# Optimization experiments

Measured on AMD Instinct MI355X. Metric: run time of the kernel, lower is better.

## Reference

```python
import jax, jax.numpy as jnp
import numpy as np

N = 1024      # number of spans
D = 512       # span embedding dim (input_dim = 3*D)
H = 150       # hidden_dim
WIN = 250     # antecedent window from spans[ix-250:ix]


def setup_inputs() -> dict:
    key = jax.random.key(0)
    ks = jax.random.split(key, 8)
    return {
        "g": jax.random.normal(ks[0], (N, D), jnp.float32),
        "sm": jax.random.normal(ks[1], (N,), jnp.float32),
        "W1": jax.random.normal(ks[2], (3 * D, H), jnp.float32) * (1.0 / np.sqrt(3 * D)),
        "b1": jax.random.normal(ks[3], (H,), jnp.float32) * 0.01,
        "W2": jax.random.normal(ks[4], (H, H), jnp.float32) * (1.0 / np.sqrt(H)),
        "b2": jax.random.normal(ks[5], (H,), jnp.float32) * 0.01,
        "W3": jax.random.normal(ks[6], (H, 1), jnp.float32) * (1.0 / np.sqrt(H)),
        "b3": jax.random.normal(ks[7], (1,), jnp.float32) * 0.01,
    }


def reference(g, sm, W1, b1, W2, b2, W3, b3):
    n, d = g.shape
    # matching the in-order iteration over spans[ix-250:ix]
    j = jnp.arange(n)[:, None] - WIN + jnp.arange(WIN)[None, :]
    valid = j >= 0
    jc = jnp.clip(j, 0)

    # pair feature is cat([g_i, g_j, g_i*g_j]); split W1 so we can factor the first GEMM
    W1a, W1b, W1c = jnp.split(W1, 3, axis=0)            # each [D, H]
    gi_term = g @ W1a                                    # [N, H]
    gj_term = (g @ W1b)[jc]
    prod_term = jnp.einsum('nwd,dh->nwh', g[:, None, :] * g[jc], W1c)

    h = jax.nn.relu(gi_term[:, None, :] + gj_term + prod_term + b1)
    h = jax.nn.relu(h @ W2 + b2)
    s = (h @ W3 + b3)[..., 0]

    sij = sm[:, None] + sm[jc] + s                       # sm_i + sm_j + s_a
    sij = jnp.where(valid, sij, 0.0)                     # mask out-of-range antecedents
    eps = jnp.zeros((n, 1), g.dtype)                     # trailing epsilon = 0
    return jnp.concatenate([sij, eps], axis=1)
```

## Files before the change

### kernel.cpp

```cpp
#include <hip/hip_runtime.h>

typedef __attribute__((ext_vector_type(8))) short short8;
typedef __attribute__((ext_vector_type(4))) float f32x4;

#define NSPAN 1024
#define DDIM  512
#define HDIM  150
#define HPAD  160
#define WINW  250
#define OUTW  251

#define B1_OFF0 0
#define B1_OFF1 10240
#define SL_OFF  40960
#define SMEM_BYTES 41472

__device__ __forceinline__ unsigned short f2bf(float x) {
  union { float f; unsigned int u; } v; v.f = x;
  return (unsigned short)((v.u + 0x7fffu + ((v.u >> 16) & 1u)) >> 16);
}

__device__ __forceinline__ unsigned int cvtpk(float a, float b) {
  unsigned int r;
  asm("v_cvt_pk_bf16_f32 %0, %1, %2" : "=v"(r) : "v"(a), "v"(b));
  return r;
}

__device__ __forceinline__ void gload_lds16(const void* g, void* l) {
  __builtin_amdgcn_global_load_lds(
      (const __attribute__((address_space(1))) unsigned int*)g,
      (__attribute__((address_space(3))) unsigned int*)l, 16, 0, 0);
}

__global__ __launch_bounds__(192) void prep_gemm(
    const float* __restrict__ g, const float* __restrict__ W1,
    const float* __restrict__ b1, float* __restrict__ pre1,
    float* __restrict__ gjb)
{
  __shared__ __align__(16) float gs[2 * DDIM];
  const int grp = blockIdx.x >> 1;
  const int which = blockIdx.x & 1;
  const int i0 = grp << 1;
  for (int idx = threadIdx.x; idx < (2 * DDIM / 4); idx += 192)
    ((float4*)gs)[idx] = ((const float4*)(g + (size_t)i0 * DDIM))[idx];
  __syncthreads();
  const int n = threadIdx.x;
  float a0 = 0.f, a1 = 0.f;
  if (n < HDIM) {
    const float* Wp = W1 + (size_t)which * DDIM * HDIM + n;
#pragma unroll 8
    for (int d = 0; d < DDIM; ++d) {
      float w = Wp[(size_t)d * HDIM];
      a0 += gs[d] * w;
      a1 += gs[DDIM + d] * w;
    }
  }
  if (n < HPAD) {
    float* dst = which ? gjb : pre1;
    float add = (which == 0 && n < HDIM) ? b1[n] : 0.f;
    float v0 = (n < HDIM) ? (a0 + add) : 0.f;
    float v1 = (n < HDIM) ? (a1 + add) : 0.f;
    dst[(size_t)i0 * HPAD + n] = v0;
    dst[(size_t)(i0 + 1) * HPAD + n] = v1;
  }
}

__global__ void prep_misc(const float* __restrict__ W1, const float* __restrict__ W2,
                          const float* __restrict__ W3,
                          unsigned short* __restrict__ w1cT,
                          unsigned short* __restrict__ w2T,
                          float* __restrict__ w3p)
{
  int id = blockIdx.x * 256 + threadIdx.x;
  if (id < HPAD * DDIM) {
    int d = id / HPAD, n = id % HPAD;
    float v = (n < HDIM) ? W1[(size_t)(2 * DDIM + d) * HDIM + n] : 0.f;
    w1cT[(size_t)n * DDIM + d] = f2bf(v);
  } else if (id < HPAD * DDIM + HPAD * HPAD) {
    int id2 = id - HPAD * DDIM;
    int k = id2 / HPAD, n = id2 % HPAD;
    float v = (n < HDIM && k < HDIM) ? W2[(size_t)k * HDIM + n] : 0.f;
    w2T[(size_t)n * HPAD + k] = f2bf(v);
  } else if (id < HPAD * DDIM + HPAD * HPAD + HPAD) {
    int n = id - HPAD * DDIM - HPAD * HPAD;
    w3p[n] = (n < HDIM) ? W3[n] : 0.f;
  }
}

__global__ __launch_bounds__(256, 3) void pair_main(
    const float* __restrict__ g, const float* __restrict__ sm,
    const float* __restrict__ pre1, const float* __restrict__ gjb,
    const unsigned short* __restrict__ w1cT, const unsigned short* __restrict__ w2T,
    const float* __restrict__ w3p, const float* __restrict__ b2,
    const float* __restrict__ b3, float* __restrict__ out)
{
  __shared__ __align__(16) char smem[SMEM_BYTES];
  const int tid = threadIdx.x;
  const int lane = tid & 63;
  const int wv = tid >> 6;
  const int l15 = lane & 15;
  const int lq = lane >> 4;
  const int i = blockIdx.x >> 1;
  const int mbase = (blockIdx.x & 1) << 7;

  const int row0 = mbase + (wv << 5) + l15;
  int j0 = i - WINW + row0;
  j0 = j0 < 0 ? 0 : (j0 > NSPAN - 1 ? NSPAN - 1 : j0);
  int j1 = i - WINW + row0 + 16;
  j1 = j1 < 0 ? 0 : (j1 > NSPAN - 1 ? NSPAN - 1 : j1);
  const float* gjr0 = g + (size_t)j0 * DDIM + (lq << 3);
  const float* gjr1 = g + (size_t)j1 * DDIM + (lq << 3);
  const float* giR  = g + (size_t)i * DDIM + (lq << 3);

  unsigned int bsrc[3];
#pragma unroll
  for (int t = 0; t < 3; ++t) {
    int b = wv * 2560 + (t << 10) + (lane << 4);
    int m = b >> 7;
    int bp = b ^ ((m & 7) << 4);
    int n = bp >> 6, o = bp & 63;
    bsrc[t] = (unsigned int)(n * 1024 + o);
  }

  int xb[10];
#pragma unroll
  for (int nt = 0; nt < 10; ++nt) {
    int nr = (nt << 4) + l15;
    xb[nt] = ((nr << 6) + (lq << 4)) ^ (((nr >> 1) & 7) << 4);
  }

  f32x4 acc[2][10];
#pragma unroll
  for (int mt = 0; mt < 2; ++mt)
#pragma unroll
    for (int nt = 0; nt < 10; ++nt)
      acc[mt][nt] = (f32x4){0.f, 0.f, 0.f, 0.f};

  const char* w1cB = (const char*)w1cT;

  {
    char* ldsw = smem + B1_OFF0 + wv * 2560;
    gload_lds16(w1cB + bsrc[0], ldsw);
    gload_lds16(w1cB + bsrc[1], ldsw + 1024);
    if (lane < 32) gload_lds16(w1cB + bsrc[2], ldsw + 2048);
  }
  uint4 aC0, aC1;
  {
    float4 x0 = *(const float4*)gjr0, x1 = *(const float4*)(gjr0 + 4);
    float4 y0 = *(const float4*)gjr1, y1 = *(const float4*)(gjr1 + 4);
    float4 g0 = *(const float4*)giR,  g1 = *(const float4*)(giR + 4);
    aC0.x = cvtpk(x0.x * g0.x, x0.y * g0.y);
    aC0.y = cvtpk(x0.z * g0.z, x0.w * g0.w);
    aC0.z = cvtpk(x1.x * g1.x, x1.y * g1.y);
    aC0.w = cvtpk(x1.z * g1.z, x1.w * g1.w);
    aC1.x = cvtpk(y0.x * g0.x, y0.y * g0.y);
    aC1.y = cvtpk(y0.z * g0.z, y0.w * g0.w);
    aC1.z = cvtpk(y1.x * g1.x, y1.y * g1.y);
    aC1.w = cvtpk(y1.z * g1.z, y1.w * g1.w);
  }
  __syncthreads();

#pragma unroll 2
  for (int s = 0; s < 16; ++s) {
    char* bcur = smem + ((s & 1) ? B1_OFF1 : B1_OFF0);
    char* bnxt = smem + ((s & 1) ? B1_OFF0 : B1_OFF1);

    if (s < 15) {
      const int kn = (s + 1) << 6;
      char* ldsw = bnxt + wv * 2560;
      gload_lds16(w1cB + bsrc[0] + kn, ldsw);
      gload_lds16(w1cB + bsrc[1] + kn, ldsw + 1024);
      if (lane < 32) gload_lds16(w1cB + bsrc[2] + kn, ldsw + 2048);
    }
    float4 x0, x1, y0, y1, g0, g1;
    if (s < 15) {
      const int kf = (s + 1) << 5;
      x0 = *(const float4*)(gjr0 + kf); x1 = *(const float4*)(gjr0 + kf + 4);
      y0 = *(const float4*)(gjr1 + kf); y1 = *(const float4*)(gjr1 + kf + 4);
      g0 = *(const float4*)(giR + kf);  g1 = *(const float4*)(giR + kf + 4);
    }
    short8 a0 = *(short8*)&aC0;
    short8 a1 = *(short8*)&aC1;
#pragma unroll
    for (int nt = 0; nt < 10; ++nt) {
      short8 bb = *(const short8*)(bcur + xb[nt]);
      acc[0][nt] = __builtin_amdgcn_mfma_f32_16x16x32_bf16(a0, bb, acc[0][nt], 0, 0, 0);
      acc[1][nt] = __builtin_amdgcn_mfma_f32_16x16x32_bf16(a1, bb, acc[1][nt], 0, 0, 0);
    }
    if (s < 15) {
      aC0.x = cvtpk(x0.x * g0.x, x0.y * g0.y);
      aC0.y = cvtpk(x0.z * g0.z, x0.w * g0.w);
      aC0.z = cvtpk(x1.x * g1.x, x1.y * g1.y);
      aC0.w = cvtpk(x1.z * g1.z, x1.w * g1.w);
      aC1.x = cvtpk(y0.x * g0.x, y0.y * g0.y);
      aC1.y = cvtpk(y0.z * g0.z, y0.w * g0.w);
      aC1.z = cvtpk(y1.x * g1.x, y1.y * g1.y);
      aC1.w = cvtpk(y1.z * g1.z, y1.w * g1.w);
    }
    __syncthreads();
  }

  float p1v[10];
#pragma unroll
  for (int nt = 0; nt < 10; ++nt)
    p1v[nt] = pre1[(size_t)i * HPAD + (nt << 4) + l15];

#pragma unroll
  for (int mt = 0; mt < 2; ++mt) {
#pragma unroll
    for (int rr = 0; rr < 4; ++rr) {
      const int row = (wv << 5) + (mt << 4) + (lq << 2) + rr;
      int j = i - WINW + mbase + row;
      j = j < 0 ? 0 : (j > NSPAN - 1 ? NSPAN - 1 : j);
      const float* gjr = gjb + (size_t)j * HPAD;
      const int sw = ((row + (row >> 2)) & 3) << 4;
      const int rb = row * 320;
#pragma unroll
      for (int np = 0; np < 5; ++np) {
        const int n0 = np << 1, n1 = n0 + 1;
        float v0 = fmaxf(acc[mt][n0][rr] + p1v[n0] + gjr[(n0 << 4) + l15], 0.f);
        float v1 = fmaxf(acc[mt][n1][rr] + p1v[n1] + gjr[(n1 << 4) + l15], 0.f);
        unsigned int u = cvtpk(v0, v1);
        *(unsigned short*)(smem + ((rb + (((n0 << 4) + l15) << 1)) ^ sw)) = (unsigned short)u;
        *(unsigned short*)(smem + ((rb + (((n1 << 4) + l15) << 1)) ^ sw)) = (unsigned short)(u >> 16);
      }
    }
  }

  int ya[2];
#pragma unroll
  for (int mt = 0; mt < 2; ++mt) {
    int row = (wv << 5) + (mt << 4) + l15;
    ya[mt] = ((row * 320) + (lq << 4)) ^ (((row + (row >> 2)) & 3) << 4);
  }

#pragma unroll
  for (int mt = 0; mt < 2; ++mt)
#pragma unroll
    for (int nt = 0; nt < 10; ++nt)
      acc[mt][nt] = (f32x4){0.f, 0.f, 0.f, 0.f};

#pragma unroll
  for (int c = 0; c < 5; ++c) {
    short8 a0 = *(const short8*)(smem + ya[0] + (c << 6));
    short8 a1 = *(const short8*)(smem + ya[1] + (c << 6));
#pragma unroll
    for (int nt = 0; nt < 10; ++nt) {
      short8 bb = *(const short8*)(w2T + (size_t)((nt << 4) + l15) * HPAD + (c << 5) + (lq << 3));
      acc[0][nt] = __builtin_amdgcn_mfma_f32_16x16x32_bf16(a0, bb, acc[0][nt], 0, 0, 0);
      acc[1][nt] = __builtin_amdgcn_mfma_f32_16x16x32_bf16(a1, bb, acc[1][nt], 0, 0, 0);
    }
  }

  float w3v[10], b2v[10];
#pragma unroll
  for (int nt = 0; nt < 10; ++nt) {
    int nn = (nt << 4) + l15;
    w3v[nt] = w3p[nn];
    b2v[nt] = (nn < HDIM) ? b2[nn] : 0.f;
  }
  float* sL = (float*)(smem + SL_OFF);
#pragma unroll
  for (int mt = 0; mt < 2; ++mt) {
#pragma unroll
    for (int rr = 0; rr < 4; ++rr) {
      float part = 0.f;
#pragma unroll
      for (int nt = 0; nt < 10; ++nt) {
        float h2 = fmaxf(acc[mt][nt][rr] + b2v[nt], 0.f);
        part = fmaf(h2, w3v[nt], part);
      }
      part += __shfl_xor(part, 1);
      part += __shfl_xor(part, 2);
      part += __shfl_xor(part, 4);
      part += __shfl_xor(part, 8);
      if (l15 == 0)
        sL[(wv << 5) + (mt << 4) + (lq << 2) + rr] = part;
    }
  }
  __syncthreads();

  if (tid < 128) {
    const int rg = mbase + tid;
    if (rg <= WINW) {
      const int j = i - WINW + rg;
      float v = 0.f;
      if (rg < WINW && j >= 0)
        v = sL[tid] + b3[0] + sm[i] + sm[j];
      out[(size_t)i * OUTW + rg] = v;
    }
  }
}

extern "C" void kernel_launch(void* const* d_in, const int* in_sizes, int n_in,
                              void* d_out, int out_size, void* d_ws, size_t ws_size,
                              hipStream_t stream) {
  const float* g  = (const float*)d_in[0];
  const float* sm = (const float*)d_in[1];
  const float* W1 = (const float*)d_in[2];
  const float* b1 = (const float*)d_in[3];
  const float* W2 = (const float*)d_in[4];
  const float* b2 = (const float*)d_in[5];
  const float* W3 = (const float*)d_in[6];
  const float* b3 = (const float*)d_in[7];
  float* out = (float*)d_out;

  char* ws = (char*)d_ws;
  float* pre1          = (float*)ws;
  float* gjb           = (float*)(ws + 655360);
  unsigned short* w1cT = (unsigned short*)(ws + 1310720);
  unsigned short* w2T  = (unsigned short*)(ws + 1474560);
  float* w3p           = (float*)(ws + 1525760);

  prep_gemm<<<1024, 192, 0, stream>>>(g, W1, b1, pre1, gjb);
  prep_misc<<<(HPAD * DDIM + HPAD * HPAD + HPAD + 255) / 256, 256, 0, stream>>>(
      W1, W2, W3, w1cT, w2T, w3p);
  pair_main<<<2048, 256, 0, stream>>>(g, sm, pre1, gjb, w1cT, w2T, w3p, b2, b3, out);
}
```

Baseline: 209.7 us.

## Read W1c B-fragments directly from global and merge prep kernels into one launch

```diff
diff --git a/kernel.cpp b/kernel.cpp
--- a/kernel.cpp
+++ b/kernel.cpp
@@ -10,8 +10,6 @@
 #define WINW  250
 #define OUTW  251
 
-#define B1_OFF0 0
-#define B1_OFF1 10240
 #define SL_OFF  40960
 #define SMEM_BYTES 41472
 
@@ -26,64 +24,55 @@
   return r;
 }
 
-__device__ __forceinline__ void gload_lds16(const void* g, void* l) {
-  __builtin_amdgcn_global_load_lds(
-      (const __attribute__((address_space(1))) unsigned int*)g,
-      (__attribute__((address_space(3))) unsigned int*)l, 16, 0, 0);
-}
-
-__global__ __launch_bounds__(192) void prep_gemm(
+__global__ __launch_bounds__(192) void prep_all(
     const float* __restrict__ g, const float* __restrict__ W1,
-    const float* __restrict__ b1, float* __restrict__ pre1,
-    float* __restrict__ gjb)
+    const float* __restrict__ b1, const float* __restrict__ W2,
+    const float* __restrict__ W3,
+    float* __restrict__ pre1, float* __restrict__ gjb,
+    unsigned short* __restrict__ w1cT, unsigned short* __restrict__ w2T,
+    float* __restrict__ w3p)
 {
-  __shared__ __align__(16) float gs[2 * DDIM];
-  const int grp = blockIdx.x >> 1;
-  const int which = blockIdx.x & 1;
-  const int i0 = grp << 1;
-  for (int idx = threadIdx.x; idx < (2 * DDIM / 4); idx += 192)
-    ((float4*)gs)[idx] = ((const float4*)(g + (size_t)i0 * DDIM))[idx];
-  __syncthreads();
-  const int n = threadIdx.x;
-  float a0 = 0.f, a1 = 0.f;
-  if (n < HDIM) {
-    const float* Wp = W1 + (size_t)which * DDIM * HDIM + n;
+  const int bx = blockIdx.x;
+  if (bx < 1024) {
+    __shared__ __align__(16) float gs[2 * DDIM];
+    const int grp = bx >> 1;
+    const int which = bx & 1;
+    const int i0 = grp << 1;
+    for (int idx = threadIdx.x; idx < (2 * DDIM / 4); idx += 192)
+      ((float4*)gs)[idx] = ((const float4*)(g + (size_t)i0 * DDIM))[idx];
+    __syncthreads();
+    const int n = threadIdx.x;
+    float a0 = 0.f, a1 = 0.f;
+    if (n < HDIM) {
+      const float* Wp = W1 + (size_t)which * DDIM * HDIM + n;
 #pragma unroll 8
-    for (int d = 0; d < DDIM; ++d) {
-      float w = Wp[(size_t)d * HDIM];
-      a0 += gs[d] * w;
-      a1 += gs[DDIM + d] * w;
-    }
-  }
-  if (n < HPAD) {
-    float* dst = which ? gjb : pre1;
-    float add = (which == 0 && n < HDIM) ? b1[n] : 0.f;
-    float v0 = (n < HDIM) ? (a0 + add) : 0.f;
-    float v1 = (n < HDIM) ? (a1 + add) : 0.f;
-    dst[(size_t)i0 * HPAD + n] = v0;
-    dst[(size_t)(i0 + 1) * HPAD + n] = v1;
-  }
-}
-
-__global__ void prep_misc(const float* __restrict__ W1, const float* __restrict__ W2,
-                          const float* __restrict__ W3,
-                          unsigned short* __restrict__ w1cT,
-                          unsigned short* __restrict__ w2T,
-                          float* __restrict__ w3p)
-{
-  int id = blockIdx.x * 256 + threadIdx.x;
-  if (id < HPAD * DDIM) {
-    int d = id / HPAD, n = id % HPAD;
-    float v = (n < HDIM) ? W1[(size_t)(2 * DDIM + d) * HDIM + n] : 0.f;
-    w1cT[(size_t)n * DDIM + d] = f2bf(v);
-  } else if (id < HPAD * DDIM + HPAD * HPAD) {
-    int id2 = id - HPAD * DDIM;
-    int k = id2 / HPAD, n = id2 % HPAD;
-    float v = (n < HDIM && k < HDIM) ? W2[(size_t)k * HDIM + n] : 0.f;
-    w2T[(size_t)n * HPAD + k] = f2bf(v);
-  } else if (id < HPAD * DDIM + HPAD * HPAD + HPAD) {
-    int n = id - HPAD * DDIM - HPAD * HPAD;
-    w3p[n] = (n < HDIM) ? W3[n] : 0.f;
+      for (int d = 0; d < DDIM; ++d) {
+        float w = Wp[(size_t)d * HDIM];
+        a0 += gs[d] * w;
+        a1 += gs[DDIM + d] * w;
+      }
+    }
+    if (n < HPAD) {
+      float* dst = which ? gjb : pre1;
+      float add = (which == 0 && n < HDIM) ? b1[n] : 0.f;
+      dst[(size_t)i0 * HPAD + n]       = (n < HDIM) ? (a0 + add) : 0.f;
+      dst[(size_t)(i0 + 1) * HPAD + n] = (n < HDIM) ? (a1 + add) : 0.f;
+    }
+  } else {
+    int id = (bx - 1024) * 192 + threadIdx.x;
+    if (id < HPAD * DDIM) {
+      int d = id / HPAD, n = id % HPAD;
+      float v = (n < HDIM) ? W1[(size_t)(2 * DDIM + d) * HDIM + n] : 0.f;
+      w1cT[(size_t)n * DDIM + d] = f2bf(v);
+    } else if (id < HPAD * DDIM + HPAD * HPAD) {
+      int id2 = id - HPAD * DDIM;
+      int k = id2 / HPAD, n = id2 % HPAD;
+      float v = (n < HDIM && k < HDIM) ? W2[(size_t)k * HDIM + n] : 0.f;
+      w2T[(size_t)n * HPAD + k] = f2bf(v);
+    } else if (id < HPAD * DDIM + HPAD * HPAD + HPAD) {
+      int n = id - HPAD * DDIM - HPAD * HPAD;
+      w3p[n] = (n < HDIM) ? W3[n] : 0.f;
+    }
   }
 }
 
@@ -112,22 +101,7 @@
   const float* gjr1 = g + (size_t)j1 * DDIM + (lq << 3);
   const float* giR  = g + (size_t)i * DDIM + (lq << 3);
 
-  unsigned int bsrc[3];
-#pragma unroll
-  for (int t = 0; t < 3; ++t) {
-    int b = wv * 2560 + (t << 10) + (lane << 4);
-    int m = b >> 7;
-    int bp = b ^ ((m & 7) << 4);
-    int n = bp >> 6, o = bp & 63;
-    bsrc[t] = (unsigned int)(n * 1024 + o);
-  }
-
-  int xb[10];
-#pragma unroll
-  for (int nt = 0; nt < 10; ++nt) {
-    int nr = (nt << 4) + l15;
-    xb[nt] = ((nr << 6) + (lq << 4)) ^ (((nr >> 1) & 7) << 4);
-  }
+  const unsigned short* bB = w1cT + (size_t)l15 * DDIM + (lq << 3);
 
   f32x4 acc[2][10];
 #pragma unroll
@@ -136,19 +110,13 @@
     for (int nt = 0; nt < 10; ++nt)
       acc[mt][nt] = (f32x4){0.f, 0.f, 0.f, 0.f};
 
-  const char* w1cB = (const char*)w1cT;
-
-  {
-    char* ldsw = smem + B1_OFF0 + wv * 2560;
-    gload_lds16(w1cB + bsrc[0], ldsw);
-    gload_lds16(w1cB + bsrc[1], ldsw + 1024);
-    if (lane < 32) gload_lds16(w1cB + bsrc[2], ldsw + 2048);
-  }
-  uint4 aC0, aC1;
-  {
-    float4 x0 = *(const float4*)gjr0, x1 = *(const float4*)(gjr0 + 4);
-    float4 y0 = *(const float4*)gjr1, y1 = *(const float4*)(gjr1 + 4);
-    float4 g0 = *(const float4*)giR,  g1 = *(const float4*)(giR + 4);
+#pragma unroll 2
+  for (int s = 0; s < 16; ++s) {
+    const int kf = s << 5;
+    float4 x0 = *(const float4*)(gjr0 + kf), x1 = *(const float4*)(gjr0 + kf + 4);
+    float4 y0 = *(const float4*)(gjr1 + kf), y1 = *(const float4*)(gjr1 + kf + 4);
+    float4 g0 = *(const float4*)(giR + kf),  g1 = *(const float4*)(giR + kf + 4);
+    uint4 aC0, aC1;
     aC0.x = cvtpk(x0.x * g0.x, x0.y * g0.y);
     aC0.y = cvtpk(x0.z * g0.z, x0.w * g0.w);
     aC0.z = cvtpk(x1.x * g1.x, x1.y * g1.y);
@@ -157,47 +125,14 @@
     aC1.y = cvtpk(y0.z * g0.z, y0.w * g0.w);
     aC1.z = cvtpk(y1.x * g1.x, y1.y * g1.y);
     aC1.w = cvtpk(y1.z * g1.z, y1.w * g1.w);
-  }
-  __syncthreads();
-
-#pragma unroll 2
-  for (int s = 0; s < 16; ++s) {
-    char* bcur = smem + ((s & 1) ? B1_OFF1 : B1_OFF0);
-    char* bnxt = smem + ((s & 1) ? B1_OFF0 : B1_OFF1);
-
-    if (s < 15) {
-      const int kn = (s + 1) << 6;
-      char* ldsw = bnxt + wv * 2560;
-      gload_lds16(w1cB + bsrc[0] + kn, ldsw);
-      gload_lds16(w1cB + bsrc[1] + kn, ldsw + 1024);
-      if (lane < 32) gload_lds16(w1cB + bsrc[2] + kn, ldsw + 2048);
-    }
-    float4 x0, x1, y0, y1, g0, g1;
-    if (s < 15) {
-      const int kf = (s + 1) << 5;
-      x0 = *(const float4*)(gjr0 + kf); x1 = *(const float4*)(gjr0 + kf + 4);
-      y0 = *(const float4*)(gjr1 + kf); y1 = *(const float4*)(gjr1 + kf + 4);
-      g0 = *(const float4*)(giR + kf);  g1 = *(const float4*)(giR + kf + 4);
-    }
     short8 a0 = *(short8*)&aC0;
     short8 a1 = *(short8*)&aC1;
 #pragma unroll
     for (int nt = 0; nt < 10; ++nt) {
-      short8 bb = *(const short8*)(bcur + xb[nt]);
+      short8 bb = *(const short8*)(bB + nt * 16 * DDIM + kf);
       acc[0][nt] = __builtin_amdgcn_mfma_f32_16x16x32_bf16(a0, bb, acc[0][nt], 0, 0, 0);
       acc[1][nt] = __builtin_amdgcn_mfma_f32_16x16x32_bf16(a1, bb, acc[1][nt], 0, 0, 0);
     }
-    if (s < 15) {
-      aC0.x = cvtpk(x0.x * g0.x, x0.y * g0.y);
-      aC0.y = cvtpk(x0.z * g0.z, x0.w * g0.w);
-      aC0.z = cvtpk(x1.x * g1.x, x1.y * g1.y);
-      aC0.w = cvtpk(x1.z * g1.z, x1.w * g1.w);
-      aC1.x = cvtpk(y0.x * g0.x, y0.y * g0.y);
-      aC1.y = cvtpk(y0.z * g0.z, y0.w * g0.w);
-      aC1.z = cvtpk(y1.x * g1.x, y1.y * g1.y);
-      aC1.w = cvtpk(y1.z * g1.z, y1.w * g1.w);
-    }
-    __syncthreads();
   }
 
   float p1v[10];
@@ -312,8 +247,6 @@
   unsigned short* w2T  = (unsigned short*)(ws + 1474560);
   float* w3p           = (float*)(ws + 1525760);
 
-  prep_gemm<<<1024, 192, 0, stream>>>(g, W1, b1, pre1, gjb);
-  prep_misc<<<(HPAD * DDIM + HPAD * HPAD + HPAD + 255) / 256, 256, 0, stream>>>(
-      W1, W2, W3, w1cT, w2T, w3p);
+  prep_all<<<1585, 192, 0, stream>>>(g, W1, b1, W2, W3, pre1, gjb, w1cT, w2T, w3p);
   pair_main<<<2048, 256, 0, stream>>>(g, sm, pre1, gjb, w1cT, w2T, w3p, b2, b3, out);
 }
```

After: 354.3 us. +69.0%, slower.

## Triple-buffer W1c LDS staging with one barrier per step and merge prep kernels

Applied to the files above, without the earlier changes.

```diff
diff --git a/kernel.cpp b/kernel.cpp
--- a/kernel.cpp
+++ b/kernel.cpp
@@ -10,8 +10,6 @@
 #define WINW  250
 #define OUTW  251
 
-#define B1_OFF0 0
-#define B1_OFF1 10240
 #define SL_OFF  40960
 #define SMEM_BYTES 41472
 
@@ -32,58 +30,55 @@
       (__attribute__((address_space(3))) unsigned int*)l, 16, 0, 0);
 }
 
-__global__ __launch_bounds__(192) void prep_gemm(
+__global__ __launch_bounds__(192) void prep_all(
     const float* __restrict__ g, const float* __restrict__ W1,
-    const float* __restrict__ b1, float* __restrict__ pre1,
-    float* __restrict__ gjb)
+    const float* __restrict__ b1, const float* __restrict__ W2,
+    const float* __restrict__ W3,
+    float* __restrict__ pre1, float* __restrict__ gjb,
+    unsigned short* __restrict__ w1cT, unsigned short* __restrict__ w2T,
+    float* __restrict__ w3p)
 {
-  __shared__ __align__(16) float gs[2 * DDIM];
-  const int grp = blockIdx.x >> 1;
-  const int which = blockIdx.x & 1;
-  const int i0 = grp << 1;
-  for (int idx = threadIdx.x; idx < (2 * DDIM / 4); idx += 192)
-    ((float4*)gs)[idx] = ((const float4*)(g + (size_t)i0 * DDIM))[idx];
-  __syncthreads();
-  const int n = threadIdx.x;
-  float a0 = 0.f, a1 = 0.f;
-  if (n < HDIM) {
-    const float* Wp = W1 + (size_t)which * DDIM * HDIM + n;
+  const int bx = blockIdx.x;
+  if (bx < 1024) {
+    __shared__ __align__(16) float gs[2 * DDIM];
+    const int grp = bx >> 1;
+    const int which = bx & 1;
+    const int i0 = grp << 1;
+    for (int idx = threadIdx.x; idx < (2 * DDIM / 4); idx += 192)
+      ((float4*)gs)[idx] = ((const float4*)(g + (size_t)i0 * DDIM))[idx];
+    __syncthreads();
+    const int n = threadIdx.x;
+    float a0 = 0.f, a1 = 0.f;
+    if (n < HDIM) {
+      const float* Wp = W1 + (size_t)which * DDIM * HDIM + n;
 #pragma unroll 8
-    for (int d = 0; d < DDIM; ++d) {
-      float w = Wp[(size_t)d * HDIM];
-      a0 += gs[d] * w;
-      a1 += gs[DDIM + d] * w;
-    }
-  }
-  if (n < HPAD) {
-    float* dst = which ? gjb : pre1;
-    float add = (which == 0 && n < HDIM) ? b1[n] : 0.f;
-    float v0 = (n < HDIM) ? (a0 + add) : 0.f;
-    float v1 = (n < HDIM) ? (a1 + add) : 0.f;
-    dst[(size_t)i0 * HPAD + n] = v0;
-    dst[(size_t)(i0 + 1) * HPAD + n] = v1;
-  }
-}
-
-__global__ void prep_misc(const float* __restrict__ W1, const float* __restrict__ W2,
-                          const float* __restrict__ W3,
-                          unsigned short* __restrict__ w1cT,
-                          unsigned short* __restrict__ w2T,
-                          float* __restrict__ w3p)
-{
-  int id = blockIdx.x * 256 + threadIdx.x;
-  if (id < HPAD * DDIM) {
-    int d = id / HPAD, n = id % HPAD;
-    float v = (n < HDIM) ? W1[(size_t)(2 * DDIM + d) * HDIM + n] : 0.f;
-    w1cT[(size_t)n * DDIM + d] = f2bf(v);
-  } else if (id < HPAD * DDIM + HPAD * HPAD) {
-    int id2 = id - HPAD * DDIM;
-    int k = id2 / HPAD, n = id2 % HPAD;
-    float v = (n < HDIM && k < HDIM) ? W2[(size_t)k * HDIM + n] : 0.f;
-    w2T[(size_t)n * HPAD + k] = f2bf(v);
-  } else if (id < HPAD * DDIM + HPAD * HPAD + HPAD) {
-    int n = id - HPAD * DDIM - HPAD * HPAD;
-    w3p[n] = (n < HDIM) ? W3[n] : 0.f;
+      for (int d = 0; d < DDIM; ++d) {
+        float w = Wp[(size_t)d * HDIM];
+        a0 += gs[d] * w;
+        a1 += gs[DDIM + d] * w;
+      }
+    }
+    if (n < HPAD) {
+      float* dst = which ? gjb : pre1;
+      float add = (which == 0 && n < HDIM) ? b1[n] : 0.f;
+      dst[(size_t)i0 * HPAD + n]       = (n < HDIM) ? (a0 + add) : 0.f;
+      dst[(size_t)(i0 + 1) * HPAD + n] = (n < HDIM) ? (a1 + add) : 0.f;
+    }
+  } else {
+    int id = (bx - 1024) * 192 + threadIdx.x;
+    if (id < HPAD * DDIM) {
+      int d = id / HPAD, n = id % HPAD;
+      float v = (n < HDIM) ? W1[(size_t)(2 * DDIM + d) * HDIM + n] : 0.f;
+      w1cT[(size_t)n * DDIM + d] = f2bf(v);
+    } else if (id < HPAD * DDIM + HPAD * HPAD) {
+      int id2 = id - HPAD * DDIM;
+      int k = id2 / HPAD, n = id2 % HPAD;
+      float v = (n < HDIM && k < HDIM) ? W2[(size_t)k * HDIM + n] : 0.f;
+      w2T[(size_t)n * HPAD + k] = f2bf(v);
+    } else if (id < HPAD * DDIM + HPAD * HPAD + HPAD) {
+      int n = id - HPAD * DDIM - HPAD * HPAD;
+      w3p[n] = (n < HDIM) ? W3[n] : 0.f;
+    }
   }
 }
 
@@ -138,17 +133,21 @@
 
   const char* w1cB = (const char*)w1cT;
 
-  {
-    char* ldsw = smem + B1_OFF0 + wv * 2560;
-    gload_lds16(w1cB + bsrc[0], ldsw);
-    gload_lds16(w1cB + bsrc[1], ldsw + 1024);
-    if (lane < 32) gload_lds16(w1cB + bsrc[2], ldsw + 2048);
-  }
+#define STAGE_B(sidx)                                                       \
+  {                                                                         \
+    char* ldsw = smem + ((sidx) % 3) * 10240 + wv * 2560;                   \
+    const int kn_ = (sidx) << 6;                                            \
+    gload_lds16(w1cB + bsrc[0] + kn_, ldsw);                                \
+    gload_lds16(w1cB + bsrc[1] + kn_, ldsw + 1024);                         \
+    if (lane < 32) gload_lds16(w1cB + bsrc[2] + kn_, ldsw + 2048);          \
+  }
+
   uint4 aC0, aC1;
   {
     float4 x0 = *(const float4*)gjr0, x1 = *(const float4*)(gjr0 + 4);
     float4 y0 = *(const float4*)gjr1, y1 = *(const float4*)(gjr1 + 4);
     float4 g0 = *(const float4*)giR,  g1 = *(const float4*)(giR + 4);
+    STAGE_B(0);
     aC0.x = cvtpk(x0.x * g0.x, x0.y * g0.y);
     aC0.y = cvtpk(x0.z * g0.z, x0.w * g0.w);
     aC0.z = cvtpk(x1.x * g1.x, x1.y * g1.y);
@@ -158,27 +157,23 @@
     aC1.z = cvtpk(y1.x * g1.x, y1.y * g1.y);
     aC1.w = cvtpk(y1.z * g1.z, y1.w * g1.w);
   }
-  __syncthreads();
-
-#pragma unroll 2
+
+#pragma unroll
   for (int s = 0; s < 16; ++s) {
-    char* bcur = smem + ((s & 1) ? B1_OFF1 : B1_OFF0);
-    char* bnxt = smem + ((s & 1) ? B1_OFF0 : B1_OFF1);
-
-    if (s < 15) {
-      const int kn = (s + 1) << 6;
-      char* ldsw = bnxt + wv * 2560;
-      gload_lds16(w1cB + bsrc[0] + kn, ldsw);
-      gload_lds16(w1cB + bsrc[1] + kn, ldsw + 1024);
-      if (lane < 32) gload_lds16(w1cB + bsrc[2] + kn, ldsw + 2048);
-    }
     float4 x0, x1, y0, y1, g0, g1;
     if (s < 15) {
       const int kf = (s + 1) << 5;
       x0 = *(const float4*)(gjr0 + kf); x1 = *(const float4*)(gjr0 + kf + 4);
       y0 = *(const float4*)(gjr1 + kf); y1 = *(const float4*)(gjr1 + kf + 4);
       g0 = *(const float4*)(giR + kf);  g1 = *(const float4*)(giR + kf + 4);
-    }
+      STAGE_B(s + 1);
+      asm volatile("s_waitcnt vmcnt(9)" ::: "memory");
+    } else {
+      asm volatile("s_waitcnt vmcnt(0)" ::: "memory");
+    }
+    __builtin_amdgcn_s_barrier();
+
+    const char* bcur = smem + (s % 3) * 10240;
     short8 a0 = *(short8*)&aC0;
     short8 a1 = *(short8*)&aC1;
 #pragma unroll
@@ -197,8 +192,9 @@
       aC1.z = cvtpk(y1.x * g1.x, y1.y * g1.y);
       aC1.w = cvtpk(y1.z * g1.z, y1.w * g1.w);
     }
-    __syncthreads();
-  }
+  }
+#undef STAGE_B
+  __syncthreads();
 
   float p1v[10];
 #pragma unroll
@@ -312,8 +308,6 @@
   unsigned short* w2T  = (unsigned short*)(ws + 1474560);
   float* w3p           = (float*)(ws + 1525760);
 
-  prep_gemm<<<1024, 192, 0, stream>>>(g, W1, b1, pre1, gjb);
-  prep_misc<<<(HPAD * DDIM + HPAD * HPAD + HPAD + 255) / 256, 256, 0, stream>>>(
-      W1, W2, W3, w1cT, w2T, w3p);
+  prep_all<<<1585, 192, 0, stream>>>(g, W1, b1, W2, W3, pre1, gjb, w1cT, w2T, w3p);
   pair_main<<<2048, 256, 0, stream>>>(g, sm, pre1, gjb, w1cT, w2T, w3p, b2, b3, out);
 }
```

Result: slower. 253.9 us (+21.1%).
